# Kernel tuning notes

Measured on AMD Instinct MI355X. Metric: run time of the kernel, lower is better.

The kernel has to match this reference:

```python
import jax, jax.numpy as jnp
import numpy as np

B, S, D, G = 16, 2048, 768, 1024  # batch, max_len, embedding_dim, groups per row (pairs)


def setup_inputs() -> dict:
    key = jax.random.key(0)
    k1, k2, k3, k4 = jax.random.split(key, 4)
    tensors_batch = jax.random.normal(k1, (B, S, D), jnp.float32)
    # ragged chunk structure encoded densely: token j belongs to group j//2 (contiguous pairs)
    group_ids = jnp.tile(jnp.arange(S, dtype=jnp.int32) // 2, (B, 1))
    padding_mask = jnp.ones((B, S), jnp.int32)  # all tokens real -> no column removal
    # masks must be constant within each group (the module asserts any()==all())
    regular_tokens_mask = jnp.repeat(jax.random.randint(k2, (B, G), 0, 2, jnp.int32), 2, axis=1)
    seq_pair_mask = jnp.repeat(jax.random.randint(k3, (B, G), 0, 2, jnp.int32), 2, axis=1)
    W = jax.random.normal(k4, (D, D), jnp.float32) / np.sqrt(D)
    b = jnp.zeros((D,), jnp.float32)
    return {
        "tensors_batch": tensors_batch,
        "group_ids": group_ids,
        "padding_mask": padding_mask,
        "regular_tokens_mask": regular_tokens_mask,
        "seq_pair_mask": seq_pair_mask,
        "num_groups": G,
        "W": W,
        "b": b,
    }


def reference(tensors_batch, group_ids, padding_mask, regular_tokens_mask, seq_pair_mask, num_groups, W, b):
    Bv, Sv, Dv = tensors_batch.shape
    Gv = num_groups
    # flatten (batch, group) into one segment axis: segment id = b*G + group
    flat_ids = (group_ids + jnp.arange(Bv, dtype=group_ids.dtype)[:, None] * Gv).reshape(-1)
    # gen_net = mean over group tokens, then Linear + tanh (applied to every group at once)
    sums = jax.ops.segment_sum(tensors_batch.reshape(Bv * Sv, Dv), flat_ids, num_segments=Bv * Gv)
    counts = jax.ops.segment_sum(jnp.ones((Bv * Sv,), tensors_batch.dtype), flat_ids, num_segments=Bv * Gv)
    mean = sums / counts[:, None]
    compact = jnp.tanh(mean @ W + b).reshape(Bv, Gv, Dv)
    # per-group mask reductions (masks are group-constant by construction)
    seg_any = lambda m: (jax.ops.segment_max(m.reshape(-1), flat_ids, num_segments=Bv * Gv) > 0)
    seg_all = lambda m: (jax.ops.segment_min(m.reshape(-1), flat_ids, num_segments=Bv * Gv) > 0)
    mask_padding = seg_any(padding_mask).astype(jnp.int32).reshape(Bv, Gv)        # sum != 0
    mask_regular = seg_any(regular_tokens_mask).astype(jnp.int32).reshape(Bv, Gv) # sum != 0
    mask_seq_pair = seg_all(seq_pair_mask).astype(jnp.int32).reshape(Bv, Gv)      # prod != 0
    mask_seq_pair = jnp.where(mask_padding == 0, jnp.int32(-1), mask_seq_pair)
    # column removal: keep columns where any batch has a real group; with all-real padding
    # every column is kept, so shapes stay static (faithful to original under these inputs)
    compression_rate = mask_regular.sum().astype(jnp.float32) / regular_tokens_mask.sum().astype(jnp.float32)
    return compact, mask_padding, mask_regular, mask_seq_pair, compression_rate
```

## Files before the change

kernel.cpp:

```cpp
#include <hip/hip_runtime.h>
#include <hip/hip_bf16.h>

#define NB 16
#define NS 2048
#define ND 768
#define NG 1024
#define ROWS (NB * NG)

#define BM 64
#define BN 256
#define BK 32
#define NCOL (ND / BN)
#define NROW (ROWS / BM)

typedef __attribute__((ext_vector_type(8))) __bf16 bf16x8;
typedef __attribute__((ext_vector_type(8))) unsigned short ushort8_t;
typedef __attribute__((ext_vector_type(4))) float f32x4;

__device__ __forceinline__ unsigned short f2bf(float f) {
    unsigned int u = __builtin_bit_cast(unsigned int, f);
    return (unsigned short)((u + 0x7FFFu + ((u >> 16) & 1u)) >> 16);
}

__device__ __forceinline__ void gload_lds16(const void* g, void* l) {
    __builtin_amdgcn_global_load_lds((const __attribute__((address_space(1))) unsigned int*)g,
                                     (__attribute__((address_space(3))) unsigned int*)l, 16, 0, 0);
}

__device__ __forceinline__ float fast_tanh(float v) {
    float x = fminf(fmaxf(v, -15.f), 15.f);
    float e = __expf(2.f * x);
    return (e - 1.f) / (e + 1.f);
}

__global__ __launch_bounds__(256) void wtrans_kernel(const float* __restrict__ W,
                                                     unsigned short* __restrict__ Bt) {
    __shared__ float tile[64][65];
    int n0 = blockIdx.x * 64;
    int k0 = blockIdx.y * 64;
    int tx = threadIdx.x & 63;
    int ty = threadIdx.x >> 6;
    #pragma unroll
    for (int i = 0; i < 64; i += 4)
        tile[ty + i][tx] = W[(long)(k0 + ty + i) * ND + n0 + tx];
    __syncthreads();
    #pragma unroll
    for (int i = 0; i < 64; i += 4)
        Bt[(long)(n0 + ty + i) * ND + k0 + tx] = f2bf(0.5f * tile[tx][ty + i]);
}

__global__ __launch_bounds__(256, 3) void gemm_fused_kernel(const float* __restrict__ x,
                                                            const unsigned short* __restrict__ Bt,
                                                            const float* __restrict__ bias,
                                                            float* __restrict__ out) {
    __shared__ unsigned short Al[BM * BK];
    __shared__ unsigned short Bl[BN * BK];
    int tid = threadIdx.x;
    int lane = tid & 63;
    int w = tid >> 6;
    int r = lane & 15, h = lane >> 4;

    int bid = blockIdx.x;
    int xcd = bid & 7;
    int s = bid >> 3;
    int c = s % 3;
    int rb = (s / 3) * 8 + xcd;
    int row0 = rb * BM;
    int col0 = c * BN;

    int b = row0 >> 10;
    long tokrow = (long)b * NS + 2 * (row0 & (NG - 1));

    int ag = w * 16 + r;
    const float* ax0 = x + (tokrow + 2 * ag) * ND + h * 8;
    const float* ax1 = ax0 + ND;
    char* alw = (char*)Al + tid * 16;

    const char* gBbase = (const char*)Bt + (long)(col0 + w * 16 + r) * (ND * 2) + h * 16;
    char* lB = (char*)Bl + tid * 16;

    float4 a0, a1, b0, b1;
    a0 = *(const float4*)ax0;  b0 = *(const float4*)(ax0 + 4);
    a1 = *(const float4*)ax1;  b1 = *(const float4*)(ax1 + 4);

    f32x4 acc[4][4] = {};

    for (int k0 = 0; k0 < ND; k0 += BK) {
        #pragma unroll
        for (int q = 0; q < 4; ++q)
            gload_lds16(gBbase + (long)q * 64 * (ND * 2) + k0 * 2, lB + q * 4096);
        ushort8_t aw;
        #pragma unroll
        for (int e = 0; e < 4; ++e) {
            aw[e]     = f2bf(a0[e] + a1[e]);
            aw[4 + e] = f2bf(b0[e] + b1[e]);
        }
        *(ushort8_t*)alw = aw;
        __syncthreads();

        int adv = (k0 + BK < ND) ? BK : 0;
        ax0 += adv; ax1 += adv;
        a0 = *(const float4*)ax0;  b0 = *(const float4*)(ax0 + 4);
        a1 = *(const float4*)ax1;  b1 = *(const float4*)(ax1 + 4);

        bf16x8 af[4];
        #pragma unroll
        for (int m = 0; m < 4; ++m)
            af[m] = __builtin_bit_cast(bf16x8, *(const ushort8_t*)((const char*)Al + m * 1024 + lane * 16));
        #pragma unroll
        for (int n = 0; n < 4; ++n) {
            bf16x8 bfv = __builtin_bit_cast(bf16x8, *(const ushort8_t*)((const char*)Bl + (w * 4 + n) * 1024 + lane * 16));
            #pragma unroll
            for (int m = 0; m < 4; ++m)
                acc[m][n] = __builtin_amdgcn_mfma_f32_16x16x32_bf16(af[m], bfv, acc[m][n], 0, 0, 0);
        }
        __syncthreads();
    }

    float bv[4];
    #pragma unroll
    for (int n = 0; n < 4; ++n) bv[n] = bias[col0 + w * 64 + n * 16 + r];

    #pragma unroll
    for (int m = 0; m < 4; ++m) {
        #pragma unroll
        for (int q = 0; q < 4; ++q) {
            int orow = row0 + m * 16 + h * 4 + q;
            float* op = out + (long)orow * ND + col0 + w * 64 + r;
            #pragma unroll
            for (int n = 0; n < 4; ++n)
                op[n * 16] = fast_tanh(acc[m][n][q] + bv[n]);
        }
    }
}

__global__ __launch_bounds__(256) void masks_kernel(const int* __restrict__ padding,
                                                    const int* __restrict__ regular,
                                                    const int* __restrict__ seqpair,
                                                    float* __restrict__ out_mp,
                                                    float* __restrict__ out_mr,
                                                    float* __restrict__ out_ms,
                                                    int2* __restrict__ partials) {
    int i = blockIdx.x * 256 + threadIdx.x;
    int b = i >> 10, g = i & (NG - 1);
    int t = b * NS + 2 * g;
    int r0 = regular[t], r1 = regular[t + 1];
    int p  = ((padding[t] | padding[t + 1]) != 0) ? 1 : 0;
    int mr = ((r0 | r1) != 0) ? 1 : 0;
    int ms = ((seqpair[t] > 0) && (seqpair[t + 1] > 0)) ? 1 : 0;
    if (p == 0) ms = -1;
    out_mp[i] = (float)p;
    out_mr[i] = (float)mr;
    out_ms[i] = (float)ms;

    int mrs = mr, tok = r0 + r1;
    #pragma unroll
    for (int off = 32; off > 0; off >>= 1) {
        mrs += __shfl_down(mrs, off);
        tok += __shfl_down(tok, off);
    }
    __shared__ int sm[4], st[4];
    int wv = threadIdx.x >> 6, lane = threadIdx.x & 63;
    if (lane == 0) { sm[wv] = mrs; st[wv] = tok; }
    __syncthreads();
    if (threadIdx.x == 0)
        partials[blockIdx.x] = make_int2(sm[0] + sm[1] + sm[2] + sm[3],
                                         st[0] + st[1] + st[2] + st[3]);
}

__global__ void cr_kernel(const int2* __restrict__ partials, float* __restrict__ cr) {
    int2 p = partials[threadIdx.x];
    int a = p.x, t = p.y;
    #pragma unroll
    for (int off = 32; off > 0; off >>= 1) {
        a += __shfl_down(a, off);
        t += __shfl_down(t, off);
    }
    if (threadIdx.x == 0) cr[0] = (float)a / (float)t;
}

extern "C" void kernel_launch(void* const* d_in, const int* in_sizes, int n_in,
                              void* d_out, int out_size, void* d_ws, size_t ws_size,
                              hipStream_t stream) {
    const float* x        = (const float*)d_in[0];
    const int*   padding  = (const int*)d_in[2];
    const int*   regular  = (const int*)d_in[3];
    const int*   seqpair  = (const int*)d_in[4];
    const float* W        = (const float*)d_in[6];
    const float* bias     = (const float*)d_in[7];

    float* outc   = (float*)d_out;
    float* out_mp = outc + (long)ROWS * ND;
    float* out_mr = out_mp + ROWS;
    float* out_ms = out_mr + ROWS;
    float* out_cr = out_ms + ROWS;

    unsigned short* wbt = (unsigned short*)d_ws;
    int2* partials = (int2*)((char*)d_ws + 1179648);

    wtrans_kernel<<<dim3(ND / 64, ND / 64), 256, 0, stream>>>(W, wbt);
    masks_kernel<<<ROWS / 256, 256, 0, stream>>>(padding, regular, seqpair, out_mp, out_mr, out_ms, partials);
    gemm_fused_kernel<<<NCOL * NROW, 256, 0, stream>>>(x, wbt, bias, outc);
    cr_kernel<<<1, 64, 0, stream>>>(partials, out_cr);
}
```

Before: 230.5 us.

## Double-buffer LDS tiles with software-pipelined loads and XOR-swizzled layout

Splits the A and B shared-memory tiles into two buffers. The B tile for step k+1 and the A registers for step k+2 are fetched while MFMAs run on step k, which leaves one barrier per k-step instead of two. The LDS layout becomes row-major with an XOR swizzle on the 16-byte chunks to reduce bank conflicts on MFMA operand reads. Manual s_waitcnt vmcnt/lgkmcnt counts replace __syncthreads. This adds register and LDS pressure and depends on the compiler keeping the memory-op order the counts assume.

```diff
diff --git a/kernel.cpp b/kernel.cpp
--- a/kernel.cpp
+++ b/kernel.cpp
@@ -12,6 +12,7 @@
 #define BK 32
 #define NCOL (ND / BN)
 #define NROW (ROWS / BM)
+#define NT (ND / BK)
 
 typedef __attribute__((ext_vector_type(8))) __bf16 bf16x8;
 typedef __attribute__((ext_vector_type(8))) unsigned short ushort8_t;
@@ -32,6 +33,9 @@
     float e = __expf(2.f * x);
     return (e - 1.f) / (e + 1.f);
 }
+
+#define VMCNT4   asm volatile("s_waitcnt vmcnt(4)" ::: "memory")
+#define LGKMCNT0 asm volatile("s_waitcnt lgkmcnt(0)" ::: "memory")
 
 __global__ __launch_bounds__(256) void wtrans_kernel(const float* __restrict__ W,
                                                      unsigned short* __restrict__ Bt) {
@@ -53,8 +57,8 @@
                                                             const unsigned short* __restrict__ Bt,
                                                             const float* __restrict__ bias,
                                                             float* __restrict__ out) {
-    __shared__ unsigned short Al[BM * BK];
-    __shared__ unsigned short Bl[BN * BK];
+    __shared__ unsigned short Al[2][BM * BK];
+    __shared__ unsigned short Bl[2][BN * BK];
     int tid = threadIdx.x;
     int lane = tid & 63;
     int w = tid >> 6;
@@ -71,50 +75,80 @@
     int b = row0 >> 10;
     long tokrow = (long)b * NS + 2 * (row0 & (NG - 1));
 
-    int ag = w * 16 + r;
-    const float* ax0 = x + (tokrow + 2 * ag) * ND + h * 8;
+    const float* ax0 = x + (tokrow + 2 * (tid >> 2)) * ND + (tid & 3) * 8;
     const float* ax1 = ax0 + ND;
-    char* alw = (char*)Al + tid * 16;
-
-    const char* gBbase = (const char*)Bt + (long)(col0 + w * 16 + r) * (ND * 2) + h * 16;
-    char* lB = (char*)Bl + tid * 16;
-
-    float4 a0, a1, b0, b1;
-    a0 = *(const float4*)ax0;  b0 = *(const float4*)(ax0 + 4);
-    a1 = *(const float4*)ax1;  b1 = *(const float4*)(ax1 + 4);
+    int swz = ((tid & 3) ^ ((tid >> 3) & 3));
+    int aw_off = (tid >> 2) * 64 + swz * 16;
+    const char* gB = (const char*)Bt + (long)(col0 + (tid >> 2)) * (ND * 2) + swz * 16;
+
+    int aoff[4], boff[4];
+    #pragma unroll
+    for (int m = 0; m < 4; ++m) {
+        int row = m * 16 + r;
+        aoff[m] = row * 64 + ((h ^ ((row >> 1) & 3)) * 16);
+    }
+    #pragma unroll
+    for (int n = 0; n < 4; ++n) {
+        int row = w * 64 + n * 16 + r;
+        boff[n] = row * 64 + ((h ^ ((row >> 1) & 3)) * 16);
+    }
 
     f32x4 acc[4][4] = {};
-
-    for (int k0 = 0; k0 < ND; k0 += BK) {
-        #pragma unroll
-        for (int q = 0; q < 4; ++q)
-            gload_lds16(gBbase + (long)q * 64 * (ND * 2) + k0 * 2, lB + q * 4096);
-        ushort8_t aw;
-        #pragma unroll
-        for (int e = 0; e < 4; ++e) {
-            aw[e]     = f2bf(a0[e] + a1[e]);
-            aw[4 + e] = f2bf(b0[e] + b1[e]);
-        }
-        *(ushort8_t*)alw = aw;
-        __syncthreads();
-
-        int adv = (k0 + BK < ND) ? BK : 0;
-        ax0 += adv; ax1 += adv;
-        a0 = *(const float4*)ax0;  b0 = *(const float4*)(ax0 + 4);
-        a1 = *(const float4*)ax1;  b1 = *(const float4*)(ax1 + 4);
-
-        bf16x8 af[4];
-        #pragma unroll
-        for (int m = 0; m < 4; ++m)
-            af[m] = __builtin_bit_cast(bf16x8, *(const ushort8_t*)((const char*)Al + m * 1024 + lane * 16));
-        #pragma unroll
-        for (int n = 0; n < 4; ++n) {
-            bf16x8 bfv = __builtin_bit_cast(bf16x8, *(const ushort8_t*)((const char*)Bl + (w * 4 + n) * 1024 + lane * 16));
-            #pragma unroll
-            for (int m = 0; m < 4; ++m)
-                acc[m][n] = __builtin_amdgcn_mfma_f32_16x16x32_bf16(af[m], bfv, acc[m][n], 0, 0, 0);
-        }
-        __syncthreads();
+    float4 a0A, a1A, b0A, b1A, a0B, a1B, b0B, b1B;
+
+#define LOADA(KT, A0, A1, B0, B1) do { \
+        const float* p0 = ax0 + (KT) * BK; const float* p1 = ax1 + (KT) * BK; \
+        A0 = *(const float4*)p0; B0 = *(const float4*)(p0 + 4); \
+        A1 = *(const float4*)p1; B1 = *(const float4*)(p1 + 4); } while (0)
+
+#define GLOADB(KT, CUR) do { \
+        const char* gb = gB + (long)(KT) * 64; \
+        _Pragma("unroll") \
+        for (int q = 0; q < 4; ++q) \
+            gload_lds16(gb + (long)q * 64 * (ND * 2), (char*)&Bl[CUR][0] + q * 4096 + tid * 16); } while (0)
+
+#define AWRITE(CUR, A0, A1, B0, B1) do { \
+        ushort8_t t8; \
+        _Pragma("unroll") \
+        for (int e = 0; e < 4; ++e) { t8[e] = f2bf(A0[e] + A1[e]); t8[4 + e] = f2bf(B0[e] + B1[e]); } \
+        *(ushort8_t*)((char*)&Al[CUR][0] + aw_off) = t8; } while (0)
+
+#define COMPUTE(CUR) do { \
+        bf16x8 af[4]; \
+        _Pragma("unroll") \
+        for (int m = 0; m < 4; ++m) \
+            af[m] = __builtin_bit_cast(bf16x8, *(const ushort8_t*)((const char*)&Al[CUR][0] + aoff[m])); \
+        _Pragma("unroll") \
+        for (int n = 0; n < 4; ++n) { \
+            bf16x8 bv = __builtin_bit_cast(bf16x8, *(const ushort8_t*)((const char*)&Bl[CUR][0] + boff[n])); \
+            _Pragma("unroll") \
+            for (int m = 0; m < 4; ++m) \
+                acc[m][n] = __builtin_amdgcn_mfma_f32_16x16x32_bf16(af[m], bv, acc[m][n], 0, 0, 0); \
+        } } while (0)
+
+#define STEP(T, CUR, LA0, LA1, LB0, LB1, UA0, UA1, UB0, UB1) do { \
+        int kb = ((T) + 1 < NT) ? (T) + 1 : NT - 1; \
+        int ka = ((T) + 2 < NT) ? (T) + 2 : NT - 1; \
+        GLOADB(kb, (CUR) ^ 1); \
+        LOADA(ka, LA0, LA1, LB0, LB1); \
+        COMPUTE(CUR); \
+        AWRITE((CUR) ^ 1, UA0, UA1, UB0, UB1);    \
+        VMCNT4;     \
+        LGKMCNT0;   \
+        __builtin_amdgcn_s_barrier(); } while (0)
+
+    LOADA(0, a0A, a1A, b0A, b1A);
+    GLOADB(0, 0);
+    AWRITE(0, a0A, a1A, b0A, b1A);
+    LOADA(1, a0B, a1B, b0B, b1B);
+    VMCNT4;
+    LGKMCNT0;
+    __builtin_amdgcn_s_barrier();
+
+    #pragma unroll 2
+    for (int t = 0; t < NT; t += 2) {
+        STEP(t,     0, a0A, a1A, b0A, b1A,  a0B, a1B, b0B, b1B);
+        STEP(t + 1, 1, a0B, a1B, b0B, b1B,  a0A, a1A, b0A, b1A);
     }
 
     float bv[4];
@@ -132,6 +166,11 @@
                 op[n * 16] = fast_tanh(acc[m][n][q] + bv[n]);
         }
     }
+#undef LOADA
+#undef GLOADB
+#undef AWRITE
+#undef COMPUTE
+#undef STEP
 }
 
 __global__ __launch_bounds__(256) void masks_kernel(const int* __restrict__ padding,
```

New measurement: 209.0 us. 9.3% less time.

## Precompute bf16 pair-means and use double-buffered swizzled 128x128 GEMM

Applied to the files above, without the earlier changes.

Moves the pair-mean and bf16 cast into a separate kernel writing a bf16 activation buffer, so the GEMM no longer reloads fp32 input for each column block. The GEMM switches to 128x128 tiles with double-buffered LDS filled by direct global-to-LDS loads, XOR-swizzled layout and explicit waitcnt pipelining. Output writes become nontemporal. This adds an extra kernel launch and a 24MB intermediate write/read in exchange.

```diff
diff --git a/kernel.cpp b/kernel.cpp
--- a/kernel.cpp
+++ b/kernel.cpp
@@ -7,11 +7,13 @@
 #define NG 1024
 #define ROWS (NB * NG)
 
-#define BM 64
-#define BN 256
+#define BM 128
+#define BN 128
 #define BK 32
-#define NCOL (ND / BN)
-#define NROW (ROWS / BM)
+#define NT (ND / BK)
+#define NCB (ND / BN)
+#define NRB (ROWS / BM)
+#define ROWSTRIDE ((long)64 * ND * 2)
 
 typedef __attribute__((ext_vector_type(8))) __bf16 bf16x8;
 typedef __attribute__((ext_vector_type(8))) unsigned short ushort8_t;
@@ -31,6 +33,30 @@
     float x = fminf(fmaxf(v, -15.f), 15.f);
     float e = __expf(2.f * x);
     return (e - 1.f) / (e + 1.f);
+}
+
+#define VMCNT4   asm volatile("s_waitcnt vmcnt(4)" ::: "memory")
+#define VMCNT0   asm volatile("s_waitcnt vmcnt(0)" ::: "memory")
+#define LGKMCNT0 asm volatile("s_waitcnt lgkmcnt(0)" ::: "memory")
+
+__global__ __launch_bounds__(256) void mean_cast_kernel(const float* __restrict__ x,
+                                                        unsigned short* __restrict__ mbf) {
+    long e = ((long)blockIdx.x * 256 + threadIdx.x) * 8;
+    int gg = (int)(e / ND);
+    int d  = (int)(e - (long)gg * ND);
+    int b = gg >> 10, g = gg & (NG - 1);
+    const float* p0 = x + ((long)(b * NS + 2 * g)) * ND + d;
+    float4 u0 = *(const float4*)p0;
+    float4 u1 = *(const float4*)(p0 + 4);
+    float4 v0 = *(const float4*)(p0 + ND);
+    float4 v1 = *(const float4*)(p0 + ND + 4);
+    ushort8_t o;
+    #pragma unroll
+    for (int j = 0; j < 4; ++j) {
+        o[j]     = f2bf(0.5f * (u0[j] + v0[j]));
+        o[4 + j] = f2bf(0.5f * (u1[j] + v1[j]));
+    }
+    *(ushort8_t*)(mbf + e) = o;
 }
 
 __global__ __launch_bounds__(256) void wtrans_kernel(const float* __restrict__ W,
@@ -46,90 +72,96 @@
     __syncthreads();
     #pragma unroll
     for (int i = 0; i < 64; i += 4)
-        Bt[(long)(n0 + ty + i) * ND + k0 + tx] = f2bf(0.5f * tile[tx][ty + i]);
-}
-
-__global__ __launch_bounds__(256, 3) void gemm_fused_kernel(const float* __restrict__ x,
-                                                            const unsigned short* __restrict__ Bt,
-                                                            const float* __restrict__ bias,
-                                                            float* __restrict__ out) {
-    __shared__ unsigned short Al[BM * BK];
-    __shared__ unsigned short Bl[BN * BK];
+        Bt[(long)(n0 + ty + i) * ND + k0 + tx] = f2bf(tile[tx][ty + i]);
+}
+
+__global__ __launch_bounds__(256, 3) void gemm_kernel(const unsigned short* __restrict__ A,
+                                                      const unsigned short* __restrict__ Bt,
+                                                      const float* __restrict__ bias,
+                                                      float* __restrict__ out) {
+    __shared__ unsigned short Al[2][BM * BK];
+    __shared__ unsigned short Bl[2][BN * BK];
     int tid = threadIdx.x;
     int lane = tid & 63;
     int w = tid >> 6;
+    int wr = w >> 1, wc = w & 1;
     int r = lane & 15, h = lane >> 4;
 
     int bid = blockIdx.x;
     int xcd = bid & 7;
     int s = bid >> 3;
-    int c = s % 3;
-    int rb = (s / 3) * 8 + xcd;
-    int row0 = rb * BM;
+    int c = s % NCB;
+    int band = (s / NCB) * 8 + xcd;
+    int row0 = band * BM;
     int col0 = c * BN;
 
-    int b = row0 >> 10;
-    long tokrow = (long)b * NS + 2 * (row0 & (NG - 1));
-
-    int ag = w * 16 + r;
-    const float* ax0 = x + (tokrow + 2 * ag) * ND + h * 8;
-    const float* ax1 = ax0 + ND;
-    char* alw = (char*)Al + tid * 16;
-
-    const char* gBbase = (const char*)Bt + (long)(col0 + w * 16 + r) * (ND * 2) + h * 16;
-    char* lB = (char*)Bl + tid * 16;
-
-    float4 a0, a1, b0, b1;
-    a0 = *(const float4*)ax0;  b0 = *(const float4*)(ax0 + 4);
-    a1 = *(const float4*)ax1;  b1 = *(const float4*)(ax1 + 4);
+    int swz = (tid & 3) ^ ((tid >> 3) & 3);
+    const char* gA = (const char*)A  + ((long)(row0 + (tid >> 2))) * (ND * 2) + swz * 16;
+    const char* gB = (const char*)Bt + ((long)(col0 + (tid >> 2))) * (ND * 2) + swz * 16;
+
+    int aoff[4], boff[4];
+    #pragma unroll
+    for (int m = 0; m < 4; ++m) {
+        int row = wr * 64 + m * 16 + r;
+        aoff[m] = row * 64 + ((h ^ ((row >> 1) & 3)) * 16);
+    }
+    #pragma unroll
+    for (int n = 0; n < 4; ++n) {
+        int row = wc * 64 + n * 16 + r;
+        boff[n] = row * 64 + ((h ^ ((row >> 1) & 3)) * 16);
+    }
+
+#define STAGE(KT, CUR) do { \
+        long kb = (long)(KT) * (BK * 2); \
+        gload_lds16(gA + kb,             (char*)&Al[CUR][0] + tid * 16); \
+        gload_lds16(gA + kb + ROWSTRIDE, (char*)&Al[CUR][0] + 4096 + tid * 16); \
+        gload_lds16(gB + kb,             (char*)&Bl[CUR][0] + tid * 16); \
+        gload_lds16(gB + kb + ROWSTRIDE, (char*)&Bl[CUR][0] + 4096 + tid * 16); \
+    } while (0)
 
     f32x4 acc[4][4] = {};
 
-    for (int k0 = 0; k0 < ND; k0 += BK) {
-        #pragma unroll
-        for (int q = 0; q < 4; ++q)
-            gload_lds16(gBbase + (long)q * 64 * (ND * 2) + k0 * 2, lB + q * 4096);
-        ushort8_t aw;
-        #pragma unroll
-        for (int e = 0; e < 4; ++e) {
-            aw[e]     = f2bf(a0[e] + a1[e]);
-            aw[4 + e] = f2bf(b0[e] + b1[e]);
+    STAGE(0, 0);
+    for (int t = 0; t < NT; ++t) {
+        int cur = t & 1;
+        LGKMCNT0;
+        __builtin_amdgcn_s_barrier();
+        if (t + 1 < NT) {
+            STAGE(t + 1, cur ^ 1);
+            VMCNT4;
+        } else {
+            VMCNT0;
         }
-        *(ushort8_t*)alw = aw;
-        __syncthreads();
-
-        int adv = (k0 + BK < ND) ? BK : 0;
-        ax0 += adv; ax1 += adv;
-        a0 = *(const float4*)ax0;  b0 = *(const float4*)(ax0 + 4);
-        a1 = *(const float4*)ax1;  b1 = *(const float4*)(ax1 + 4);
-
+        __builtin_amdgcn_s_barrier();
+        const char* ab = (const char*)&Al[cur][0];
+        const char* bb = (const char*)&Bl[cur][0];
         bf16x8 af[4];
         #pragma unroll
         for (int m = 0; m < 4; ++m)
-            af[m] = __builtin_bit_cast(bf16x8, *(const ushort8_t*)((const char*)Al + m * 1024 + lane * 16));
+            af[m] = __builtin_bit_cast(bf16x8, *(const ushort8_t*)(ab + aoff[m]));
         #pragma unroll
         for (int n = 0; n < 4; ++n) {
-            bf16x8 bfv = __builtin_bit_cast(bf16x8, *(const ushort8_t*)((const char*)Bl + (w * 4 + n) * 1024 + lane * 16));
+            bf16x8 bv = __builtin_bit_cast(bf16x8, *(const ushort8_t*)(bb + boff[n]));
             #pragma unroll
             for (int m = 0; m < 4; ++m)
-                acc[m][n] = __builtin_amdgcn_mfma_f32_16x16x32_bf16(af[m], bfv, acc[m][n], 0, 0, 0);
+                acc[m][n] = __builtin_amdgcn_mfma_f32_16x16x32_bf16(af[m], bv, acc[m][n], 0, 0, 0);
         }
-        __syncthreads();
-    }
+    }
+#undef STAGE
 
     float bv[4];
     #pragma unroll
-    for (int n = 0; n < 4; ++n) bv[n] = bias[col0 + w * 64 + n * 16 + r];
+    for (int n = 0; n < 4; ++n) bv[n] = bias[col0 + wc * 64 + n * 16 + r];
 
     #pragma unroll
     for (int m = 0; m < 4; ++m) {
         #pragma unroll
         for (int q = 0; q < 4; ++q) {
-            int orow = row0 + m * 16 + h * 4 + q;
-            float* op = out + (long)orow * ND + col0 + w * 64 + r;
+            int orow = row0 + wr * 64 + m * 16 + h * 4 + q;
+            float* op = out + (long)orow * ND + col0 + wc * 64 + r;
             #pragma unroll
             for (int n = 0; n < 4; ++n)
-                op[n * 16] = fast_tanh(acc[m][n][q] + bv[n]);
+                __builtin_nontemporal_store(fast_tanh(acc[m][n][q] + bv[n]), op + n * 16);
         }
     }
 }
@@ -195,11 +227,13 @@
     float* out_ms = out_mr + ROWS;
     float* out_cr = out_ms + ROWS;
 
-    unsigned short* wbt = (unsigned short*)d_ws;
-    int2* partials = (int2*)((char*)d_ws + 1179648);
+    unsigned short* mbf = (unsigned short*)d_ws;
+    unsigned short* wbt = (unsigned short*)((char*)d_ws + 25165824);
+    int2* partials = (int2*)((char*)d_ws + 25165824 + 1179648);
 
     wtrans_kernel<<<dim3(ND / 64, ND / 64), 256, 0, stream>>>(W, wbt);
+    mean_cast_kernel<<<(int)(((long)ROWS * ND / 8) / 256), 256, 0, stream>>>(x, mbf);
     masks_kernel<<<ROWS / 256, 256, 0, stream>>>(padding, regular, seqpair, out_mp, out_mr, out_ms, partials);
-    gemm_fused_kernel<<<NCOL * NROW, 256, 0, stream>>>(x, wbt, bias, outc);
+    gemm_kernel<<<NCB * NRB, 256, 0, stream>>>(mbf, wbt, bias, outc);
     cr_kernel<<<1, 64, 0, stream>>>(partials, out_cr);
 }
```

New measurement: 210.4 us. -8.7%, faster.
